# Kernel tuning notes

Hardware: AMD Instinct MI355X
Metric: run time of the kernel (lower is better)

The kernel has to match this reference:

```python
import jax, jax.numpy as jnp
from jax import lax
import numpy as np

B, N, D = 32, 8192, 256
EPS = 1e-06        # module eps
NUM = 1e-06        # numerator epsilon in tan_theta
BN_EPS = 1e-05     # torch BatchNorm1d default
SLOPE = 0.2        # LeakyReLU negative_slope

REG = jnp.array([[-1, -1, -1, 0, 0, 0, 1, 1, 1],
                 [-1,  0,  1, -1, 0, 1, -1, 0, 1]], dtype=jnp.float32)  # [2,9]


def conv1d(x, w, b):
    # x: [B,C,N], w: [O,C,3], pad=1 -> [B,O,N]
    y = lax.conv_general_dilated(x, w, (1,), [(1, 1)],
                                 dimension_numbers=('NCH', 'OIH', 'NCH'))
    return y + b[None, :, None]


def batchnorm(x, gamma, beta):
    # training-mode BatchNorm1d over (B, N) per channel, biased variance
    m = x.mean(axis=(0, 2), keepdims=True)
    v = ((x - m) ** 2).mean(axis=(0, 2), keepdims=True)
    return gamma[None, :, None] * (x - m) * lax.rsqrt(v + BN_EPS) + beta[None, :, None]


def setup_inputs() -> dict:
    key = jax.random.key(0)
    ks = jax.random.split(key, 12)
    s = 0.05
    return {
        'pts':      jax.random.normal(ks[0], (B, 2, N), jnp.float32),
        'feats':    jax.random.normal(ks[1], (B, D, N), jnp.float32),
        'rot_w':    jax.random.normal(ks[2], (4, D, 3), jnp.float32) * s,
        'rot_b':    jax.random.normal(ks[3], (4,), jnp.float32) * s,
        'trans_w':  jax.random.normal(ks[4], (2, D, 3), jnp.float32) * s,
        'trans_b':  jax.random.normal(ks[5], (2,), jnp.float32) * s,
        'pos_w':    jax.random.normal(ks[6], (2, 20, 3), jnp.float32) * s,
        'pos_b':    jax.random.normal(ks[7], (2,), jnp.float32) * s,
        'pos_g':    jnp.ones((2,), jnp.float32),
        'pos_beta': jnp.zeros((2,), jnp.float32),
        'ori_w':    jax.random.normal(ks[8], (2, 2, 3), jnp.float32) * s,
        'ori_b':    jax.random.normal(ks[9], (2,), jnp.float32) * s,
        'ori_g':    jnp.ones((2,), jnp.float32),
        'ori_beta': jnp.zeros((2,), jnp.float32),
    }


def compute_offset(feats, rot_w, rot_b, trans_w, trans_b):
    b, _, n = feats.shape
    tm = conv1d(feats, rot_w, rot_b)                       # [B,4,N]
    tm = tm.transpose(0, 2, 1).reshape(b, n, 2, 2)         # per-point 2x2
    transformed = jnp.einsum('bnij,jk->bnik', tm, REG)     # [B,N,2,9]
    offset = transformed - REG                             # broadcast [2,9]
    # transpose(1,2).reshape(B,N,18).permute -> interleaved (x0,y0,x1,y1,...)
    offset = offset.transpose(0, 1, 3, 2).reshape(b, n, 18).transpose(0, 2, 1)  # [B,18,N]
    translation = conv1d(feats, trans_w, trans_b)          # [B,2,N]
    # even channels += tx, odd channels += ty
    off = offset.reshape(b, 9, 2, n) + translation[:, None, :, :]
    return off.reshape(b, 18, n)


def reference(pts, feats, rot_w, rot_b, trans_w, trans_b,
              pos_w, pos_b, pos_g, pos_beta,
              ori_w, ori_b, ori_g, ori_beta):
    b, _, n = pts.shape
    offset = compute_offset(feats, rot_w, rot_b, trans_w, trans_b)  # [B,18,N]

    # geo_position branch
    x = jnp.concatenate([pts, offset], axis=1)             # [B,20,N]
    x = conv1d(x, pos_w, pos_b)                            # [B,2,N]
    x = batchnorm(x, pos_g, pos_beta)
    x = jnp.where(x >= 0, x, SLOPE * x)                    # LeakyReLU(0.2)

    # geo_orientation branch
    off_x = offset[:, 0::2, :]                             # [B,9,N]
    off_y = offset[:, 1::2, :]
    rad = jnp.arctan((off_y + NUM) / (off_x + EPS))        # [B,9,N]
    main_rad = rad.max(axis=1)                             # [B,N]
    c, s = jnp.cos(main_rad), jnp.sin(main_rad)
    # rotation[b,n] = [[cos, sin], [-sin, cos]]
    rot = jnp.stack([jnp.stack([c, s], -1), jnp.stack([-s, c], -1)], -2)  # [B,N,2,2]
    x = jnp.einsum('bxn,bnxy->byn', x, rot)                # rotate 2-d coords
    x = conv1d(x, ori_w, ori_b)
    x = batchnorm(x, ori_g, ori_beta)
    return x
```

## Files before the change

kernel.cpp:

```cpp
#include <hip/hip_runtime.h>
#include <math.h>

#define NPTS 8192
#define DCH  256
#define BB   32
#define TOTPT (BB * NPTS)

#define X1_OFF    0
#define COS_OFF   (X1_OFF + BB * 2 * NPTS)
#define SIN_OFF   (COS_OFF + TOTPT)
#define X5_OFF    (SIN_OFF + TOTPT)
#define STATS_OFF (X5_OFF + BB * 2 * NPTS)

__device__ __forceinline__ void block_reduce_atomic4(float v0, float v1,
                                                     float v2, float v3,
                                                     float* dst)
{
#pragma unroll
    for (int off = 32; off > 0; off >>= 1) {
        v0 += __shfl_down(v0, off, 64);
        v1 += __shfl_down(v1, off, 64);
        v2 += __shfl_down(v2, off, 64);
        v3 += __shfl_down(v3, off, 64);
    }
    __shared__ float red[4][4];
    const int wave = threadIdx.x >> 6, lane = threadIdx.x & 63;
    if (lane == 0) {
        red[wave][0] = v0; red[wave][1] = v1; red[wave][2] = v2; red[wave][3] = v3;
    }
    __syncthreads();
    if (threadIdx.x == 0) {
        float a0 = 0, a1 = 0, a2 = 0, a3 = 0;
#pragma unroll
        for (int w = 0; w < 4; ++w) {
            a0 += red[w][0]; a1 += red[w][1]; a2 += red[w][2]; a3 += red[w][3];
        }
        atomicAdd(dst + 0, a0); atomicAdd(dst + 1, a1);
        atomicAdd(dst + 2, a2); atomicAdd(dst + 3, a3);
    }
}

__global__ __launch_bounds__(256) void kernAB(
    const float* __restrict__ pts, const float* __restrict__ feats,
    const float* __restrict__ rot_w, const float* __restrict__ rot_b,
    const float* __restrict__ trans_w, const float* __restrict__ trans_b,
    const float* __restrict__ pos_w, const float* __restrict__ pos_b,
    float* __restrict__ x1, float* __restrict__ cosA, float* __restrict__ sinA,
    float* __restrict__ stats)
{
    const int blk  = blockIdx.x;
    const int b    = blk >> 5;
    const int n0   = (blk & 31) << 8;
    const int tid  = threadIdx.x;
    const int wave = tid >> 6;
    const int lane = tid & 63;
    const int p    = n0 + (lane << 2);

    const float* fb = feats + (size_t)b * DCH * NPTS;

    __shared__ float red[3][64][25];
    __shared__ float hw4[4][12];
    __shared__ float Tsh[6][260];

    float acc[6][4];
#pragma unroll
    for (int o = 0; o < 6; ++o)
#pragma unroll
        for (int j = 0; j < 4; ++j) acc[o][j] = 0.0f;

    const int c0 = __builtin_amdgcn_readfirstlane(wave << 6);

    const float lmask = (p > 0) ? 1.0f : 0.0f;
    const int   lidx  = (p > 0) ? (p - 1) : 0;
    const float rmask = (p + 4 < NPTS) ? 1.0f : 0.0f;
    const int   ridx  = (p + 4 < NPTS) ? (p + 4) : 0;

    const float* fr = fb + (size_t)c0 * NPTS;

#pragma unroll 4
    for (int cc = 0; cc < 64; ++cc) {
        const int c = c0 + cc;
        const float4 v = *(const float4*)(fr + p);
        const float fl = fr[lidx] * lmask;
        const float fd = fr[ridx] * rmask;
        const float f[6] = { fl, v.x, v.y, v.z, v.w, fd };
#pragma unroll
        for (int o = 0; o < 6; ++o) {
            const float* wp = (o < 4) ? (rot_w + ((size_t)o * DCH + c) * 3)
                                      : (trans_w + ((size_t)(o - 4) * DCH + c) * 3);
            const float w0 = wp[0], w1 = wp[1], w2 = wp[2];
#pragma unroll
            for (int j = 0; j < 4; ++j)
                acc[o][j] += w0 * f[j] + w1 * f[j + 1] + w2 * f[j + 2];
        }
        fr += NPTS;
    }

    float hh[12];
    {
        const float* fc = fb + (size_t)tid * NPTS;
        const int iA = (n0 >= 2) ? (n0 - 2) : 0;
        const int iB = (n0 >= 1) ? (n0 - 1) : 0;
        const float a0 = fc[iA], a1 = fc[iB], a2 = fc[n0];
        const int jB = (n0 + 256 <= NPTS - 1) ? (n0 + 256) : (NPTS - 1);
        const int jC = (n0 + 257 <= NPTS - 1) ? (n0 + 257) : (NPTS - 1);
        const float b0 = fc[n0 + 255], b1 = fc[jB], b2 = fc[jC];
#pragma unroll
        for (int o = 0; o < 6; ++o) {
            const float* wp = (o < 4) ? (rot_w + ((size_t)o * DCH + tid) * 3)
                                      : (trans_w + ((size_t)(o - 4) * DCH + tid) * 3);
            const float w0 = wp[0], w1 = wp[1], w2 = wp[2];
            hh[o]     = w0 * a0 + w1 * a1 + w2 * a2;
            hh[6 + o] = w0 * b0 + w1 * b1 + w2 * b2;
        }
    }
#pragma unroll
    for (int off = 32; off > 0; off >>= 1)
#pragma unroll
        for (int j = 0; j < 12; ++j)
            hh[j] += __shfl_down(hh[j], off, 64);

    if (wave >= 1) {
#pragma unroll
        for (int o = 0; o < 6; ++o)
#pragma unroll
            for (int j = 0; j < 4; ++j)
                red[wave - 1][lane][o * 4 + j] = acc[o][j];
    }
    if (lane == 0) {
#pragma unroll
        for (int j = 0; j < 12; ++j) hw4[wave][j] = hh[j];
    }
    __syncthreads();

    if (wave == 0) {
#pragma unroll
        for (int q = 0; q < 3; ++q)
#pragma unroll
            for (int o = 0; o < 6; ++o)
#pragma unroll
                for (int j = 0; j < 4; ++j)
                    acc[o][j] += red[q][lane][o * 4 + j];
#pragma unroll
        for (int o = 0; o < 6; ++o) {
            const float bias = (o < 4) ? rot_b[o] : trans_b[o - 4];
#pragma unroll
            for (int j = 0; j < 4; ++j)
                Tsh[o][1 + (lane << 2) + j] = acc[o][j] + bias;
        }
    }
    if (tid < 12) {
        const int o = tid % 6, side = tid / 6;
        float v = hw4[0][tid] + hw4[1][tid] + hw4[2][tid] + hw4[3][tid];
        v += (o < 4) ? rot_b[o] : trans_b[o - 4];
        Tsh[o][side ? 257 : 0] = v;
    }
    __syncthreads();

    const int n = n0 + tid;
    float tm[6][3];
#pragma unroll
    for (int o = 0; o < 6; ++o)
#pragma unroll
        for (int k = 0; k < 3; ++k)
            tm[o][k] = Tsh[o][tid + k];

    float xs0 = pos_b[0], xs1 = pos_b[1];
    float mz = -INFINITY;

#pragma unroll
    for (int m3 = 0; m3 < 3; ++m3) {
        const int m   = n + m3 - 1;
        const float msk = (m >= 0 && m < NPTS) ? 1.0f : 0.0f;
        const int mc  = (m < 0) ? 0 : ((m >= NPTS) ? NPTS - 1 : m);

        const float pa = pts[((size_t)b * 2 + 0) * NPTS + mc];
        const float pb = pts[((size_t)b * 2 + 1) * NPTS + mc];

        const float o0 = tm[0][m3] - 1.0f, o1 = tm[1][m3];
        const float o2 = tm[2][m3],        o3 = tm[3][m3] - 1.0f;
        const float tr0 = tm[4][m3],       tr1 = tm[5][m3];

        float p0 = pos_w[0 * 60 + 0 * 3 + m3] * pa + pos_w[0 * 60 + 1 * 3 + m3] * pb;
        float p1 = pos_w[1 * 60 + 0 * 3 + m3] * pa + pos_w[1 * 60 + 1 * 3 + m3] * pb;
#pragma unroll
        for (int k = 0; k < 9; ++k) {
            const float R0 = (float)(k / 3 - 1);
            const float R1 = (float)(k % 3 - 1);
            const float cx = o0 * R0 + o1 * R1 + tr0;
            const float cy = o2 * R0 + o3 * R1 + tr1;
            p0 += pos_w[0 * 60 + (2 + 2 * k) * 3 + m3] * cx
                + pos_w[0 * 60 + (3 + 2 * k) * 3 + m3] * cy;
            p1 += pos_w[1 * 60 + (2 + 2 * k) * 3 + m3] * cx
                + pos_w[1 * 60 + (3 + 2 * k) * 3 + m3] * cy;
            if (m3 == 1) {
                const float z = (cy + 1e-6f) / (cx + 1e-6f);
                mz = fmaxf(mz, z);
            }
        }
        xs0 += msk * p0;
        xs1 += msk * p1;
    }

    const float mr = atanf(mz);
    float sv, cv;
    sincosf(mr, &sv, &cv);

    const int g = (b << 13) + n;
    x1[((size_t)b * 2 + 0) * NPTS + n] = xs0;
    x1[((size_t)b * 2 + 1) * NPTS + n] = xs1;
    cosA[g] = cv;
    sinA[g] = sv;

    block_reduce_atomic4(xs0, xs1, xs0 * xs0, xs1 * xs1,
                         stats + ((blk & 15) << 2));
}

__global__ __launch_bounds__(256) void kernD(
    const float* __restrict__ x1,
    const float* __restrict__ cosA, const float* __restrict__ sinA,
    const float* __restrict__ pos_g, const float* __restrict__ pos_beta,
    const float* __restrict__ ori_w, const float* __restrict__ ori_b,
    float* __restrict__ stats, float* __restrict__ x5)
{
    const int gg = blockIdx.x * 256 + threadIdx.x;
    const int b = gg >> 13;
    const int n = gg & (NPTS - 1);

    float s0 = 0, s1 = 0, s2 = 0, s3 = 0;
#pragma unroll
    for (int q = 0; q < 16; ++q) {
        s0 += stats[q * 4 + 0]; s1 += stats[q * 4 + 1];
        s2 += stats[q * 4 + 2]; s3 += stats[q * 4 + 3];
    }
    const float cntInv = 1.0f / (float)TOTPT;
    const float m0 = s0 * cntInv, m1 = s1 * cntInv;
    const float var0 = s2 * cntInv - m0 * m0;
    const float var1 = s3 * cntInv - m1 * m1;
    const float i0 = rsqrtf(var0 + 1e-5f), i1 = rsqrtf(var1 + 1e-5f);
    const float g0 = pos_g[0], g1 = pos_g[1];
    const float be0 = pos_beta[0], be1 = pos_beta[1];

    float x4a[3], x4b[3];
#pragma unroll
    for (int m3 = 0; m3 < 3; ++m3) {
        const int m   = n + m3 - 1;
        const float msk = (m >= 0 && m < NPTS) ? 1.0f : 0.0f;
        const int mc  = (m < 0) ? 0 : ((m >= NPTS) ? NPTS - 1 : m);
        float y0 = x1[((size_t)b * 2 + 0) * NPTS + mc];
        float y1 = x1[((size_t)b * 2 + 1) * NPTS + mc];
        y0 = g0 * (y0 - m0) * i0 + be0;
        y1 = g1 * (y1 - m1) * i1 + be1;
        y0 = (y0 >= 0.0f) ? y0 : 0.2f * y0;
        y1 = (y1 >= 0.0f) ? y1 : 0.2f * y1;
        const float cv = cosA[(b << 13) + mc];
        const float sv = sinA[(b << 13) + mc];
        x4a[m3] = (y0 * cv - y1 * sv) * msk;
        x4b[m3] = (y0 * sv + y1 * cv) * msk;
    }

    float z0 = ori_b[0], z1 = ori_b[1];
#pragma unroll
    for (int k = 0; k < 3; ++k) {
        z0 += ori_w[0 * 6 + 0 * 3 + k] * x4a[k] + ori_w[0 * 6 + 1 * 3 + k] * x4b[k];
        z1 += ori_w[1 * 6 + 0 * 3 + k] * x4a[k] + ori_w[1 * 6 + 1 * 3 + k] * x4b[k];
    }
    x5[((size_t)b * 2 + 0) * NPTS + n] = z0;
    x5[((size_t)b * 2 + 1) * NPTS + n] = z1;

    block_reduce_atomic4(z0, z1, z0 * z0, z1 * z1,
                         stats + 64 + ((blockIdx.x & 15) << 2));
}

__global__ __launch_bounds__(256) void kernE(
    const float* __restrict__ x5, const float* __restrict__ stats,
    const float* __restrict__ ori_g, const float* __restrict__ ori_beta,
    float* __restrict__ out)
{
    const int gg = blockIdx.x * 256 + threadIdx.x;
    const int o = (gg >> 13) & 1;
    float sm = 0, sq = 0;
#pragma unroll
    for (int q = 0; q < 16; ++q) {
        sm += stats[64 + q * 4 + o];
        sq += stats[64 + q * 4 + 2 + o];
    }
    const float cntInv = 1.0f / (float)TOTPT;
    const float m  = sm * cntInv;
    const float vv = sq * cntInv - m * m;
    const float inv = rsqrtf(vv + 1e-5f);
    out[gg] = ori_g[o] * (x5[gg] - m) * inv + ori_beta[o];
}

extern "C" void kernel_launch(void* const* d_in, const int* in_sizes, int n_in,
                              void* d_out, int out_size, void* d_ws, size_t ws_size,
                              hipStream_t stream)
{
    const float* pts      = (const float*)d_in[0];
    const float* feats    = (const float*)d_in[1];
    const float* rot_w    = (const float*)d_in[2];
    const float* rot_b    = (const float*)d_in[3];
    const float* trans_w  = (const float*)d_in[4];
    const float* trans_b  = (const float*)d_in[5];
    const float* pos_w    = (const float*)d_in[6];
    const float* pos_b    = (const float*)d_in[7];
    const float* pos_g    = (const float*)d_in[8];
    const float* pos_beta = (const float*)d_in[9];
    const float* ori_w    = (const float*)d_in[10];
    const float* ori_b    = (const float*)d_in[11];
    const float* ori_g    = (const float*)d_in[12];
    const float* ori_beta = (const float*)d_in[13];

    float* ws    = (float*)d_ws;
    float* x1    = ws + X1_OFF;
    float* cosA  = ws + COS_OFF;
    float* sinA  = ws + SIN_OFF;
    float* x5    = ws + X5_OFF;
    float* stats = ws + STATS_OFF;

    hipMemsetAsync(stats, 0, 128 * sizeof(float), stream);

    kernAB<<<1024, 256, 0, stream>>>(pts, feats, rot_w, rot_b, trans_w, trans_b,
                                     pos_w, pos_b, x1, cosA, sinA, stats);
    kernD<<<1024, 256, 0, stream>>>(x1, cosA, sinA, pos_g, pos_beta,
                                    ori_w, ori_b, stats, x5);
    kernE<<<2048, 256, 0, stream>>>(x5, stats, ori_g, ori_beta, (float*)d_out);
}
```

Baseline: 497.6 us.

## Stage conv weights in LDS and batch feature loads eight channels deep

```diff
diff --git a/kernel.cpp b/kernel.cpp
--- a/kernel.cpp
+++ b/kernel.cpp
@@ -40,7 +40,7 @@
     }
 }
 
-__global__ __launch_bounds__(256) void kernAB(
+__global__ __launch_bounds__(256, 4) void kernAB(
     const float* __restrict__ pts, const float* __restrict__ feats,
     const float* __restrict__ rot_w, const float* __restrict__ rot_b,
     const float* __restrict__ trans_w, const float* __restrict__ trans_b,
@@ -58,9 +58,21 @@
 
     const float* fb = feats + (size_t)b * DCH * NPTS;
 
-    __shared__ float red[3][64][25];
+    __shared__ __align__(16) float shmem[5120];
     __shared__ float hw4[4][12];
     __shared__ float Tsh[6][260];
+
+    float (*wsh)[20] = (float (*)[20])shmem;
+
+    for (int i = tid; i < 4608; i += 256) {
+        float v;
+        int o, r;
+        if (i < 3072) { v = rot_w[i];          o = i / 768;              r = i % 768; }
+        else          { v = trans_w[i - 3072]; o = 4 + (i - 3072) / 768; r = (i - 3072) % 768; }
+        const int c = r / 3, k = r % 3;
+        wsh[c][o * 3 + k] = v;
+    }
+    __syncthreads();
 
     float acc[6][4];
 #pragma unroll
@@ -77,23 +89,33 @@
 
     const float* fr = fb + (size_t)c0 * NPTS;
 
-#pragma unroll 4
-    for (int cc = 0; cc < 64; ++cc) {
-        const int c = c0 + cc;
-        const float4 v = *(const float4*)(fr + p);
-        const float fl = fr[lidx] * lmask;
-        const float fd = fr[ridx] * rmask;
-        const float f[6] = { fl, v.x, v.y, v.z, v.w, fd };
-#pragma unroll
-        for (int o = 0; o < 6; ++o) {
-            const float* wp = (o < 4) ? (rot_w + ((size_t)o * DCH + c) * 3)
-                                      : (trans_w + ((size_t)(o - 4) * DCH + c) * 3);
-            const float w0 = wp[0], w1 = wp[1], w2 = wp[2];
-#pragma unroll
-            for (int j = 0; j < 4; ++j)
-                acc[o][j] += w0 * f[j] + w1 * f[j + 1] + w2 * f[j + 2];
-        }
-        fr += NPTS;
+#pragma unroll 1
+    for (int base = 0; base < 64; base += 8) {
+        float4 v[8]; float fl[8], fd[8];
+#pragma unroll
+        for (int u = 0; u < 8; ++u) {
+            const float* frc = fr + (size_t)u * NPTS;
+            v[u]  = *(const float4*)(frc + p);
+            fl[u] = frc[lidx] * lmask;
+            fd[u] = frc[ridx] * rmask;
+        }
+#pragma unroll
+        for (int u = 0; u < 8; ++u) {
+            const float* wr = wsh[c0 + base + u];
+            float w[18];
+            *(float4*)(w + 0)  = *(const float4*)(wr + 0);
+            *(float4*)(w + 4)  = *(const float4*)(wr + 4);
+            *(float4*)(w + 8)  = *(const float4*)(wr + 8);
+            *(float4*)(w + 12) = *(const float4*)(wr + 12);
+            *(float2*)(w + 16) = *(const float2*)(wr + 16);
+            const float f[6] = { fl[u], v[u].x, v[u].y, v[u].z, v[u].w, fd[u] };
+#pragma unroll
+            for (int o = 0; o < 6; ++o)
+#pragma unroll
+                for (int j = 0; j < 4; ++j)
+                    acc[o][j] += w[o * 3] * f[j] + w[o * 3 + 1] * f[j + 1] + w[o * 3 + 2] * f[j + 2];
+        }
+        fr += (size_t)8 * NPTS;
     }
 
     float hh[12];
@@ -105,11 +127,10 @@
         const int jB = (n0 + 256 <= NPTS - 1) ? (n0 + 256) : (NPTS - 1);
         const int jC = (n0 + 257 <= NPTS - 1) ? (n0 + 257) : (NPTS - 1);
         const float b0 = fc[n0 + 255], b1 = fc[jB], b2 = fc[jC];
+        const float* wr = wsh[tid];
 #pragma unroll
         for (int o = 0; o < 6; ++o) {
-            const float* wp = (o < 4) ? (rot_w + ((size_t)o * DCH + tid) * 3)
-                                      : (trans_w + ((size_t)(o - 4) * DCH + tid) * 3);
-            const float w0 = wp[0], w1 = wp[1], w2 = wp[2];
+            const float w0 = wr[o * 3], w1 = wr[o * 3 + 1], w2 = wr[o * 3 + 2];
             hh[o]     = w0 * a0 + w1 * a1 + w2 * a2;
             hh[6 + o] = w0 * b0 + w1 * b1 + w2 * b2;
         }
@@ -119,6 +140,9 @@
 #pragma unroll
         for (int j = 0; j < 12; ++j)
             hh[j] += __shfl_down(hh[j], off, 64);
+
+    __syncthreads();
+    float (*red)[64][25] = (float (*)[64][25])shmem;
 
     if (wave >= 1) {
 #pragma unroll
```

Measured after the change: 869.6 us. +74.7%, slower.
